# Kernel tuning notes

Hardware: AMD Instinct MI355X
Metric: run time of the kernel (lower is better)

The kernel has to match this reference:

```python
import jax, jax.numpy as jnp
import numpy as np
import math

B, S, D, H, DH, DFF = 2, 2048, 2048, 16, 128, 8192
EPS = 1e-6
K_AMB = -1.0


def log_map_origin(x, K):
    # x: (..., d+1) Lorentz point -> tangent vector (..., d)
    xi = x[..., 1:]
    n = jnp.sqrt(jnp.sum(xi * xi, axis=-1, keepdims=True))
    a = jnp.sqrt(-K) * n
    # asinh(a)/a, stable near 0 (on-manifold, acosh(sqrt(-K)x0) == asinh(sqrt(-K)||xi||))
    f = jnp.where(a < 1e-6, 1.0 - a * a / 6.0, jnp.arcsinh(a) / jnp.maximum(a, 1e-12))
    return f * xi


def exp_map_stable(v, K):
    # v: (..., d) tangent -> Lorentz point (..., d+1); x0 from exact constraint
    n = jnp.sqrt(jnp.sum(v * v, axis=-1, keepdims=True))
    a = jnp.sqrt(-K) * n
    sinc = jnp.where(a < 1e-6, 1.0 + a * a / 6.0, jnp.sinh(a) / jnp.maximum(a, 1e-12))
    xi = sinc * v
    x0 = jnp.sqrt(-1.0 / K + jnp.sum(xi * xi, axis=-1, keepdims=True))
    return jnp.concatenate([x0, xi], axis=-1)


def lorentz_rmsnorm(x, scale):
    v = log_map_origin(x, K_AMB)
    rms = jnp.sqrt(jnp.mean(v * v, axis=-1, keepdims=True) + EPS)
    return exp_map_stable(scale * (v / rms), K_AMB)


def per_head_attention(x_normed, mask, Wq, Wk, Wv, Wo, head_K):
    v = log_map_origin(x_normed, K_AMB)  # (B,S,D)
    def split(w):
        return (v @ w).reshape(B, S, H, DH).transpose(0, 2, 1, 3)  # (B,H,S,DH)
    q, k, vv = split(Wq), split(Wk), split(Wv)
    Kh = head_K[None, :, None, None]  # (1,H,1,1) per-head curvature
    ql = exp_map_stable(q, Kh)  # (B,H,S,DH+1)
    kl = exp_map_stable(k, Kh)
    # Lorentz inner product <q,k>_L = -q0 k0 + qi.ki via signed metric
    metric = jnp.concatenate([-jnp.ones((1,)), jnp.ones((DH,))])
    L = jnp.einsum('bhqd,bhkd->bhqk', ql * metric, kl)
    # negative squared-distance proxy: 2<q,k>_L - 2/K  (zero when q==k)
    scores = (2.0 * L - 2.0 / Kh) / math.sqrt(DH)
    scores = jnp.where(mask[None, None, :, :], scores, -1e30)
    attn = jax.nn.softmax(scores, axis=-1)
    out = jnp.einsum('bhqk,bhkd->bhqd', attn, vv)  # (B,H,S,DH)
    out = out.transpose(0, 2, 1, 3).reshape(B, S, H * DH)
    return out @ Wo  # Euclidean (B,S,D)


def block_forward(x, mask, scale1, scale2, Wq, Wk, Wv, Wo, head_K, W1, W2):
    xn = lorentz_rmsnorm(x, scale1)
    attn_out = per_head_attention(xn, mask, Wq, Wk, Wv, Wo, head_K)
    x = exp_map_stable(log_map_origin(x, K_AMB) + attn_out, K_AMB)
    xn = lorentz_rmsnorm(x, scale2)
    vf = log_map_origin(xn, K_AMB)
    ffn_eu_pre = jax.nn.gelu(vf @ W1, approximate=False) @ W2
    ffn_out = exp_map_stable(ffn_eu_pre, K_AMB)
    x = exp_map_stable(log_map_origin(x, K_AMB) + log_map_origin(ffn_out, K_AMB), K_AMB)
    return x


def setup_inputs() -> dict:
    key = jax.random.key(0)
    ks = jax.random.split(key, 9)
    v0 = jax.random.normal(ks[0], (B, S, D), jnp.float32) * 0.02
    x = exp_map_stable(v0, K_AMB)  # on-manifold input (B,S,D+1)
    mask = jnp.tril(jnp.ones((S, S), bool))  # causal: True = attend
    init_scale = 1.0 / math.sqrt(D)
    w_std = 0.02
    return {
        'x': x,
        'mask': mask,
        'scale1': jnp.full((D,), init_scale, jnp.float32),
        'scale2': jnp.full((D,), init_scale, jnp.float32),
        'Wq': jax.random.normal(ks[1], (D, H * DH), jnp.float32) * w_std,
        'Wk': jax.random.normal(ks[2], (D, H * DH), jnp.float32) * w_std,
        'Wv': jax.random.normal(ks[3], (D, H * DH), jnp.float32) * w_std,
        'Wo': jax.random.normal(ks[4], (H * DH, D), jnp.float32) * w_std,
        'head_K': jnp.full((H,), -1.0, jnp.float32),
        'W1': jax.random.normal(ks[5], (D, DFF), jnp.float32) * w_std,
        'W2': jax.random.normal(ks[6], (DFF, D), jnp.float32) * w_std,
    }


def reference(x, mask, scale1, scale2, Wq, Wk, Wv, Wo, head_K, W1, W2):
    return block_forward(x, mask, scale1, scale2, Wq, Wk, Wv, Wo, head_K, W1, W2)
```

## Files before the change

### kernel.cpp

```cpp
#include <hip/hip_runtime.h>
#include <stdint.h>

typedef unsigned short u16;
typedef __attribute__((ext_vector_type(8))) short bf16x8;
typedef __attribute__((ext_vector_type(4))) float f32x4;

#define SEQ    2048
#define NB     2
#define NHEAD  16
#define DHEAD  128
#define DMODEL 2048
#define DFFN   8192
#define MROWS  4096

__device__ __forceinline__ u16 f2bf(float x) {
  union { float f; uint32_t u; } v; v.f = x;
  return (u16)((v.u + 0x7fffu + ((v.u >> 16) & 1u)) >> 16);
}
__device__ __forceinline__ float bf2f(u16 h) {
  union { uint32_t u; float f; } v; v.u = ((uint32_t)h) << 16;
  return v.f;
}
__device__ __forceinline__ void gload16(const void* g, void* l) {
  __builtin_amdgcn_global_load_lds((const __attribute__((address_space(1))) void*)g,
                                   (__attribute__((address_space(3))) void*)l,
                                   16, 0, 0);
}
__device__ __forceinline__ float blockSum256(float v) {
  __shared__ float red[4];
  #pragma unroll
  for (int m = 1; m < 64; m <<= 1) v += __shfl_xor(v, m, 64);
  int w = threadIdx.x >> 6;
  if ((threadIdx.x & 63) == 0) red[w] = v;
  __syncthreads();
  float s = red[0] + red[1] + red[2] + red[3];
  __syncthreads();
  return s;
}

__global__ void transpose_w(const float* __restrict__ in, u16* __restrict__ out, int R, int C) {
  __shared__ float tile[32][33];
  int c0 = blockIdx.x * 32, r0 = blockIdx.y * 32;
  int tx = threadIdx.x, ty = threadIdx.y;
  #pragma unroll
  for (int i = 0; i < 4; ++i)
    tile[ty + 8*i][tx] = in[(size_t)(r0 + ty + 8*i) * C + c0 + tx];
  __syncthreads();
  #pragma unroll
  for (int i = 0; i < 4; ++i)
    out[(size_t)(c0 + ty + 8*i) * R + r0 + tx] = f2bf(tile[tx][ty + 8*i]);
}

__global__ void ln_first(const float* __restrict__ x, const float* __restrict__ scale,
                         float* __restrict__ v1, u16* __restrict__ t1) {
  int row = blockIdx.x;
  const float* xr = x + (size_t)row * (DMODEL + 1) + 1;
  float vals[8]; float ss = 0.f;
  #pragma unroll
  for (int i = 0; i < 8; ++i) {
    int idx = threadIdx.x + 256 * i;
    vals[i] = xr[idx];
    ss += vals[i] * vals[i];
  }
  ss = blockSum256(ss);
  float n = sqrtf(ss);
  float f = (n < 1e-6f) ? (1.0f - n * n * (1.0f/6.0f)) : (asinhf(n) / n);
  float rms = sqrtf(f * f * ss * (1.0f / DMODEL) + 1e-6f);
  float ir = 1.0f / rms;
  #pragma unroll
  for (int i = 0; i < 8; ++i) {
    int idx = threadIdx.x + 256 * i;
    float v = f * vals[i];
    v1[(size_t)row * DMODEL + idx] = v;
    t1[(size_t)row * DMODEL + idx] = f2bf(scale[idx] * v * ir);
  }
}

__global__ void rms_mid3(float* __restrict__ u, const float* __restrict__ p0,
                         const float* __restrict__ p1, const float* __restrict__ scale,
                         u16* __restrict__ t) {
  int row = blockIdx.x;
  size_t base = (size_t)row * DMODEL;
  float vals[8]; float ss = 0.f;
  #pragma unroll
  for (int i = 0; i < 8; ++i) {
    int idx = threadIdx.x + 256*i;
    float v = u[base + idx] + p0[base + idx] + p1[base + idx];
    vals[i] = v; ss += v*v;
  }
  ss = blockSum256(ss);
  float ir = 1.0f / sqrtf(ss * (1.0f / DMODEL) + 1e-6f);
  #pragma unroll
  for (int i = 0; i < 8; ++i) {
    int idx = threadIdx.x + 256*i;
    u[base + idx] = vals[i];
    t[base + idx] = f2bf(scale[idx]*vals[i]*ir);
  }
}

__global__ void final_exp3(const float* __restrict__ u, const float* __restrict__ p0,
                           const float* __restrict__ p1, float* __restrict__ out) {
  int row = blockIdx.x;
  size_t base = (size_t)row * DMODEL;
  float vals[8]; float ss = 0.f;
  #pragma unroll
  for (int i = 0; i < 8; ++i) {
    int idx = threadIdx.x + 256*i;
    float v = u[base + idx] + p0[base + idx] + p1[base + idx];
    vals[i] = v; ss += v*v;
  }
  ss = blockSum256(ss);
  float n = sqrtf(ss);
  float f = (n < 1e-6f) ? (1.0f + n*n*(1.0f/6.0f)) : (sinhf(n)/n);
  float* orow = out + (size_t)row * (DMODEL + 1);
  if (threadIdx.x == 0) orow[0] = sqrtf(1.0f + f*f*ss);
  #pragma unroll
  for (int i = 0; i < 8; ++i) { int idx = threadIdx.x + 256*i; orow[1+idx] = f*vals[i]; }
}

template<int EPI>
__global__ __launch_bounds__(512, 2) void gemm256(
    const u16* __restrict__ A, const u16* __restrict__ Bt,
    u16* __restrict__ Cb, float* Cf,
    int M, int N, int K, int kHalf)
{
  __shared__ __attribute__((aligned(128))) char smem[131072];
  const int tid = threadIdx.x;
  const int w = tid >> 6, lane = tid & 63;
  const int lrow = lane & 15, kq = lane >> 4;
  const int wm = w >> 2, wn = w & 3;

  const int ksel = blockIdx.y;
  A  += (size_t)ksel * kHalf;
  Bt += (size_t)ksel * kHalf;
  if (EPI == 3) Cf += (size_t)ksel * M * N;
  const int NT = kHalf >> 6;

  const int nwg = gridDim.x;
  const int cpx = nwg >> 3;
  const int sid = (blockIdx.x & 7) * cpx + (blockIdx.x >> 3);
  const int NX = N >> 8;
  const int bx = sid % NX, by = sid / NX;
  const int m0 = by * 256, n0 = bx * 256;

  size_t goff[2];
  #pragma unroll
  for (int r = 0; r < 2; ++r) {
    int L = r * 8192 + tid * 16;
    int U = L ^ (((L >> 9) & 1) << 5);
    int si = U >> 10;
    int row = (si >> 1) * 16 + ((U >> 6) & 15);
    int col = (si & 1) * 32 + ((U & 63) >> 1);
    goff[r] = (size_t)row * K + col;
  }
  auto stage_half = [&](const u16* g, int ldsOff) {
    #pragma unroll
    for (int r = 0; r < 2; ++r)
      gload16(g + goff[r], smem + ldsOff + r * 8192 + w * 1024);
  };

  const u16* A0 = A  + (size_t)m0 * K;
  const u16* A1 = A  + (size_t)(m0 + 128) * K;
  const u16* B0 = Bt + (size_t)n0 * K;
  const u16* B1 = Bt + (size_t)(n0 + 128) * K;

  const int aoff = (lrow * 64 + kq * 16) ^ ((lrow & 8) << 2);

  f32x4 acc[8][4] = {};

  stage_half(A0, 0);
  stage_half(A1, 16384);
  stage_half(B0, 32768);
  stage_half(B1, 49152);
  stage_half(A0 + 64, 65536);
  stage_half(A1 + 64, 65536 + 16384);
  asm volatile("s_waitcnt vmcnt(4)" ::: "memory");
  asm volatile("s_barrier" ::: "memory");

  for (int t = 0; t < NT; ++t) {
    const int buf = t & 1;
    const char* ab = smem + buf * 65536 + wm * 16384 + aoff;
    const char* bb = smem + buf * 65536 + 32768 + (wn >> 1) * 16384 + (wn & 1) * 8192 + aoff;
    bf16x8 a0[4][2], a1[4][2], b0[2][2], b1[2][2];

    #pragma unroll
    for (int i = 0; i < 4; ++i)
      #pragma unroll
      for (int kk = 0; kk < 2; ++kk)
        a0[i][kk] = *(const bf16x8*)(ab + (i*2 + kk) * 1024);
    #pragma unroll
    for (int j = 0; j < 2; ++j)
      #pragma unroll
      for (int kk = 0; kk < 2; ++kk)
        b0[j][kk] = *(const bf16x8*)(bb + (j*2 + kk) * 1024);
    if (t + 1 < NT) stage_half(B0 + (t+1)*64, (buf^1)*65536 + 32768);
    asm volatile("s_barrier" ::: "memory");
    __builtin_amdgcn_s_setprio(1);
    #pragma unroll
    for (int kk = 0; kk < 2; ++kk)
      #pragma unroll
      for (int i = 0; i < 4; ++i)
        #pragma unroll
        for (int j = 0; j < 2; ++j)
          acc[i][j] = __builtin_amdgcn_mfma_f32_16x16x32_bf16(a0[i][kk], b0[j][kk], acc[i][j], 0, 0, 0);
    __builtin_amdgcn_s_setprio(0);
    asm volatile("s_barrier" ::: "memory");

    #pragma unroll
    for (int i = 0; i < 4; ++i)
      #pragma unroll
      for (int kk = 0; kk < 2; ++kk)
        a1[i][kk] = *(const bf16x8*)(ab + ((4 + i)*2 + kk) * 1024);
    if (t + 1 < NT) stage_half(B1 + (t+1)*64, (buf^1)*65536 + 49152);
    asm volatile("s_barrier" ::: "memory");
    __builtin_amdgcn_s_setprio(1);
    #pragma unroll
    for (int kk = 0; kk < 2; ++kk)
      #pragma unroll
      for (int i = 0; i < 4; ++i)
        #pragma unroll
        for (int j = 0; j < 2; ++j)
          acc[4 + i][j] = __builtin_amdgcn_mfma_f32_16x16x32_bf16(a1[i][kk], b0[j][kk], acc[4 + i][j], 0, 0, 0);
    __builtin_amdgcn_s_setprio(0);
    asm volatile("s_barrier" ::: "memory");

    #pragma unroll
    for (int j = 0; j < 2; ++j)
      #pragma unroll
      for (int kk = 0; kk < 2; ++kk)
        b1[j][kk] = *(const bf16x8*)(bb + ((2 + j)*2 + kk) * 1024);
    if (t + 2 < NT) stage_half(A0 + (t+2)*64, buf*65536);
    asm volatile("s_barrier" ::: "memory");
    __builtin_amdgcn_s_setprio(1);
    #pragma unroll
    for (int kk = 0; kk < 2; ++kk)
      #pragma unroll
      for (int i = 0; i < 4; ++i)
        #pragma unroll
        for (int j = 0; j < 2; ++j)
          acc[4 + i][2 + j] = __builtin_amdgcn_mfma_f32_16x16x32_bf16(a1[i][kk], b1[j][kk], acc[4 + i][2 + j], 0, 0, 0);
    __builtin_amdgcn_s_setprio(0);
    asm volatile("s_barrier" ::: "memory");

    if (t + 2 < NT) stage_half(A1 + (t+2)*64, buf*65536 + 16384);
    asm volatile("s_barrier" ::: "memory");
    __builtin_amdgcn_s_setprio(1);
    #pragma unroll
    for (int kk = 0; kk < 2; ++kk)
      #pragma unroll
      for (int i = 0; i < 4; ++i)
        #pragma unroll
        for (int j = 0; j < 2; ++j)
          acc[i][2 + j] = __builtin_amdgcn_mfma_f32_16x16x32_bf16(a0[i][kk], b1[j][kk], acc[i][2 + j], 0, 0, 0);
    __builtin_amdgcn_s_setprio(0);
    if (t + 2 < NT) asm volatile("s_waitcnt vmcnt(4)" ::: "memory");
    else            asm volatile("s_waitcnt vmcnt(0)" ::: "memory");
    asm volatile("s_barrier" ::: "memory");
  }

  #pragma unroll
  for (int i = 0; i < 8; ++i)
    #pragma unroll
    for (int j = 0; j < 4; ++j)
      #pragma unroll
      for (int r = 0; r < 4; ++r) {
        int row = m0 + wm*128 + i*16 + kq*4 + r;
        int col = n0 + wn*64 + j*16 + lrow;
        size_t idx = (size_t)row * N + col;
        float v = acc[i][j][r];
        if (EPI == 0) {
          Cb[idx] = f2bf(v);
        } else if (EPI == 3) {
          Cf[idx] = v;
        } else {
          float g = 0.5f * v * (1.0f + erff(v * 0.70710678118654752f));
          Cb[idx] = f2bf(g);
        }
      }
}

__global__ void prep_qk(const u16* __restrict__ in, const float* __restrict__ headK,
                        u16* __restrict__ Lout, float* __restrict__ l0,
                        int instride, int off) {
  int gid = blockIdx.x * 4 + (threadIdx.x >> 6);
  int lane = threadIdx.x & 63;
  int b = gid >> 15;
  int rem = gid & 32767;
  int h = rem >> 11;
  int s = rem & 2047;
  const u16* src = in + ((size_t)(b * SEQ + s)) * instride + off + h * DHEAD + lane * 2;
  float v0 = bf2f(src[0]), v1 = bf2f(src[1]);
  float nn = v0*v0 + v1*v1;
  #pragma unroll
  for (int m = 1; m < 64; m <<= 1) nn += __shfl_xor(nn, m, 64);
  float Kh = headK[h];
  float sk = sqrtf(-Kh);
  float a = sk * sqrtf(nn);
  float f = (a < 1e-6f) ? (1.0f + a*a*(1.0f/6.0f)) : (sinhf(a) / a);
  u16* dst = Lout + (size_t)gid * DHEAD + lane * 2;
  dst[0] = f2bf(f * v0);
  dst[1] = f2bf(f * v1);
  if (lane == 0) l0[gid] = sqrtf(-1.0f/Kh + f*f*nn);
}

__global__ void vtrans(const u16* __restrict__ vb, u16* __restrict__ VT,
                       int instride, int off) {
  __shared__ u16 tile[32][33];
  int bh = blockIdx.x;
  int b = bh >> 4, h = bh & 15;
  int s0 = blockIdx.y * 32, d0 = blockIdx.z * 32;
  int tx = threadIdx.x, ty = threadIdx.y;
  #pragma unroll
  for (int i = 0; i < 4; ++i)
    tile[ty + 8*i][tx] = vb[((size_t)(b*SEQ + s0 + ty + 8*i)) * instride + off + h*DHEAD + d0 + tx];
  __syncthreads();
  #pragma unroll
  for (int i = 0; i < 4; ++i)
    VT[((size_t)bh*DHEAD + d0 + ty + 8*i) * SEQ + s0 + tx] = tile[tx][ty + 8*i];
}

__global__ __launch_bounds__(256, 2) void attn_kernel(
    const u16* __restrict__ Ql, const u16* __restrict__ Kl,
    const u16* __restrict__ VT, const float* __restrict__ ql0,
    const float* __restrict__ kl0, const float* __restrict__ headK,
    u16* __restrict__ out) {
  __shared__ u16 klds[2][32 * 128];
  __shared__ u16 vlds[2][128 * 32];
  __shared__ u16 plds[4][32 * 36];
  const int tid = threadIdx.x, w = tid >> 6, lane = tid & 63;
  const int lrow = lane & 15, kq = lane >> 4;
  const int id = blockIdx.x;
  const int bh = id & 31;
  const int qb = 15 - (id >> 5);
  const int q0 = qb * 128 + w * 32;
  const int b = bh >> 4, h = bh & 15;
  const float Kh = headK[h];
  const float LOG2E = 1.44269504088896f;
  const float isd = 0.088388347648318447f;
  const float sc_mul = 2.0f * isd * LOG2E;
  const float sc_add = (-2.0f / Kh) * isd * LOG2E;

  const u16* kbase  = Kl + (size_t)bh * SEQ * DHEAD;
  const u16* vtbase = VT + (size_t)bh * DHEAD * SEQ;
  const float* kl0b = kl0 + (size_t)bh * SEQ;
  u16* pw = &plds[w][0];

  bf16x8 aq[2][4];
  const u16* qbase = Ql + ((size_t)bh * SEQ + q0) * DHEAD;
  #pragma unroll
  for (int m = 0; m < 2; ++m)
    #pragma unroll
    for (int dc = 0; dc < 4; ++dc)
      aq[m][dc] = *(const bf16x8*)&qbase[(size_t)(m*16 + lrow) * DHEAD + dc*32 + kq*8];
  float q0r[2][4];
  #pragma unroll
  for (int m = 0; m < 2; ++m)
    #pragma unroll
    for (int r = 0; r < 4; ++r)
      q0r[m][r] = ql0[(size_t)bh * SEQ + q0 + m*16 + kq*4 + r];

  auto stage = [&](int k0, int buf) {
    #pragma unroll
    for (int i = 0; i < 2; ++i) {
      int rl = w*8 + i*4 + (lane >> 4);
      int c = (lane & 15) ^ (rl & 15);
      gload16(kbase + ((size_t)(k0 + rl)) * DHEAD + c * 8,
              &klds[buf][(w*8 + i*4) * 128]);
    }
    #pragma unroll
    for (int i = 0; i < 2; ++i) {
      int rl = w*32 + i*16 + (lane >> 2);
      int c = (lane & 3) ^ ((rl >> 1) & 3);
      gload16(vtbase + (size_t)rl * SEQ + k0 + c * 8,
              &vlds[buf][(w*32 + i*16) * 32]);
    }
  };

  float lacc[2][4] = {};
  f32x4 o[2][8] = {};
  const int niter = qb * 4 + 4;

  stage(0, 0);
  for (int i = 0; i < niter; ++i) {
    const int k0 = i * 32, buf = i & 1;
    float kc0 = kl0b[k0 + lrow];
    float kc1 = kl0b[k0 + 16 + lrow];
    if (i + 1 < niter) {
      stage(k0 + 32, buf ^ 1);
      asm volatile("s_waitcnt vmcnt(4)" ::: "memory");
    } else {
      asm volatile("s_waitcnt vmcnt(0)" ::: "memory");
    }
    asm volatile("s_barrier" ::: "memory");

    f32x4 sc[2][2] = {};
    #pragma unroll
    for (int dc = 0; dc < 4; ++dc) {
      int c = dc*4 + kq;
      bf16x8 bk0 = *(const bf16x8*)&klds[buf][lrow*128        + (c ^ (lrow & 15)) * 8];
      bf16x8 bk1 = *(const bf16x8*)&klds[buf][(16 + lrow)*128 + (c ^ ((16 + lrow) & 15)) * 8];
      #pragma unroll
      for (int m = 0; m < 2; ++m) {
        sc[m][0] = __builtin_amdgcn_mfma_f32_16x16x32_bf16(aq[m][dc], bk0, sc[m][0], 0, 0, 0);
        sc[m][1] = __builtin_amdgcn_mfma_f32_16x16x32_bf16(aq[m][dc], bk1, sc[m][1], 0, 0, 0);
      }
    }
    #pragma unroll
    for (int m = 0; m < 2; ++m)
      #pragma unroll
      for (int r = 0; r < 4; ++r) {
        int qg = q0 + m*16 + kq*4 + r;
        float p0 = exp2f((sc[m][0][r] - q0r[m][r] * kc0) * sc_mul + sc_add);
        float p1 = exp2f((sc[m][1][r] - q0r[m][r] * kc1) * sc_mul + sc_add);
        p0 = (k0 + lrow      <= qg) ? p0 : 0.f;
        p1 = (k0 + 16 + lrow <= qg) ? p1 : 0.f;
        lacc[m][r] += p0 + p1;
        pw[(m*16 + kq*4 + r) * 36 + lrow]      = f2bf(p0);
        pw[(m*16 + kq*4 + r) * 36 + 16 + lrow] = f2bf(p1);
      }
    bf16x8 ap0 = *(const bf16x8*)&pw[(size_t)lrow * 36 + kq*8];
    bf16x8 ap1 = *(const bf16x8*)&pw[(size_t)(16 + lrow) * 36 + kq*8];
    int vc = (kq ^ ((lrow >> 1) & 3)) * 8;
    #pragma unroll
    for (int n = 0; n < 8; ++n) {
      bf16x8 bv = *(const bf16x8*)&vlds[buf][(n*16 + lrow) * 32 + vc];
      o[0][n] = __builtin_amdgcn_mfma_f32_16x16x32_bf16(ap0, bv, o[0][n], 0, 0, 0);
      o[1][n] = __builtin_amdgcn_mfma_f32_16x16x32_bf16(ap1, bv, o[1][n], 0, 0, 0);
    }
    asm volatile("s_barrier" ::: "memory");
  }

  float rcl[2][4];
  #pragma unroll
  for (int m = 0; m < 2; ++m)
    #pragma unroll
    for (int r = 0; r < 4; ++r) {
      float s = lacc[m][r];
      #pragma unroll
      for (int mm = 1; mm < 16; mm <<= 1) s += __shfl_xor(s, mm, 16);
      rcl[m][r] = 1.0f / s;
    }
  #pragma unroll
  for (int m = 0; m < 2; ++m)
    #pragma unroll
    for (int n = 0; n < 8; ++n)
      #pragma unroll
      for (int r = 0; r < 4; ++r) {
        int qg = q0 + m*16 + kq*4 + r;
        out[((size_t)b * SEQ + qg) * DMODEL + h * DHEAD + n*16 + lrow] =
            f2bf(o[m][n][r] * rcl[m][r]);
      }
}

extern "C" void kernel_launch(void* const* d_in, const int* in_sizes, int n_in,
                              void* d_out, int out_size, void* d_ws, size_t ws_size,
                              hipStream_t stream) {
  const float* x      = (const float*)d_in[0];
  const float* scale1 = (const float*)d_in[2];
  const float* scale2 = (const float*)d_in[3];
  const float* Wq     = (const float*)d_in[4];
  const float* Wk     = (const float*)d_in[5];
  const float* Wv     = (const float*)d_in[6];
  const float* Wo     = (const float*)d_in[7];
  const float* headK  = (const float*)d_in[8];
  const float* W1     = (const float*)d_in[9];
  const float* W2     = (const float*)d_in[10];
  float* out = (float*)d_out;

  char* p = (char*)d_ws;
  size_t off = 0;
  auto take = [&](size_t bytes) -> char* {
    char* r = p + off;
    off += (bytes + 255) & ~(size_t)255;
    return r;
  };
  u16* WqT = (u16*)take((size_t)DMODEL*DMODEL*2);
  u16* WkT = (u16*)take((size_t)DMODEL*DMODEL*2);
  u16* WvT = (u16*)take((size_t)DMODEL*DMODEL*2);
  u16* WoT = (u16*)take((size_t)DMODEL*DMODEL*2);
  u16* W1T = (u16*)take((size_t)DMODEL*DFFN*2);
  u16* W2T = (u16*)take((size_t)DMODEL*DFFN*2);
  float* vres = (float*)take((size_t)MROWS*DMODEL*4);
  u16* tbuf = (u16*)take((size_t)MROWS*DMODEL*2);
  u16* qkvb = (u16*)take((size_t)MROWS*3*DMODEL*2);
  u16* Qlb  = (u16*)take((size_t)MROWS*DMODEL*2);
  u16* Klb  = (u16*)take((size_t)MROWS*DMODEL*2);
  u16* VTb  = (u16*)take((size_t)MROWS*DMODEL*2);
  float* q0b = (float*)take((size_t)NB*NHEAD*SEQ*4);
  float* k0b = (float*)take((size_t)NB*NHEAD*SEQ*4);
  u16* hbuf = qkvb;
  u16* attnout = tbuf;

  float* PoA = (float*)qkvb;
  float* PoB = PoA + (size_t)MROWS*DMODEL;
  float* PfA = (float*)WqT;
  float* PfB = (float*)Klb;

  dim3 tb(32, 8);
  transpose_w<<<dim3(DMODEL/32, DMODEL/32), tb, 0, stream>>>(Wq, WqT, DMODEL, DMODEL);
  transpose_w<<<dim3(DMODEL/32, DMODEL/32), tb, 0, stream>>>(Wk, WkT, DMODEL, DMODEL);
  transpose_w<<<dim3(DMODEL/32, DMODEL/32), tb, 0, stream>>>(Wv, WvT, DMODEL, DMODEL);
  transpose_w<<<dim3(DMODEL/32, DMODEL/32), tb, 0, stream>>>(Wo, WoT, DMODEL, DMODEL);
  transpose_w<<<dim3(DFFN/32,   DMODEL/32), tb, 0, stream>>>(W1, W1T, DMODEL, DFFN);
  transpose_w<<<dim3(DMODEL/32, DFFN/32),   tb, 0, stream>>>(W2, W2T, DFFN, DMODEL);

  ln_first<<<MROWS, 256, 0, stream>>>(x, scale1, vres, tbuf);

  gemm256<0><<<dim3((3*DMODEL/256)*(MROWS/256), 1), 512, 0, stream>>>(
      tbuf, WqT, qkvb, nullptr, MROWS, 3*DMODEL, DMODEL, DMODEL);

  prep_qk<<<NB*NHEAD*SEQ/4, 256, 0, stream>>>(qkvb, headK, Qlb, q0b, 3*DMODEL, 0);
  prep_qk<<<NB*NHEAD*SEQ/4, 256, 0, stream>>>(qkvb, headK, Klb, k0b, 3*DMODEL, DMODEL);
  vtrans<<<dim3(NB*NHEAD, SEQ/32, DHEAD/32), tb, 0, stream>>>(qkvb, VTb, 3*DMODEL, 2*DMODEL);

  attn_kernel<<<dim3(512), 256, 0, stream>>>(Qlb, Klb, VTb, q0b, k0b, headK, attnout);

  gemm256<3><<<dim3((DMODEL/256)*(MROWS/256), 2), 512, 0, stream>>>(
      attnout, WoT, nullptr, PoA, MROWS, DMODEL, DMODEL, DMODEL/2);

  rms_mid3<<<MROWS, 256, 0, stream>>>(vres, PoA, PoB, scale2, tbuf);

  gemm256<2><<<dim3((DFFN/256)*(MROWS/256), 1), 512, 0, stream>>>(
      tbuf, W1T, hbuf, nullptr, MROWS, DFFN, DMODEL, DMODEL);

  gemm256<3><<<dim3((DMODEL/256)*(MROWS/256), 2), 512, 0, stream>>>(
      hbuf, W2T, nullptr, PfA, MROWS, DMODEL, DFFN, DFFN/2);

  final_exp3<<<MROWS, 256, 0, stream>>>(vres, PfA, (float*)W1T, out);

  (void)PfB; (void)in_sizes; (void)n_in; (void)out_size; (void)ws_size;
}
```

Baseline: 905.1 us.

## Software-pipeline GEMM LDS fragment loads across iterations and cut barriers

The bf16 MFMA GEMM main loop is restructured so the next tile's a0/b0 register fragments are read from LDS at the end of the current iteration. The first fragments are preloaded before the loop. The four MFMA quadrants are reordered (a0·b0, a0·b1, a1·b0, a1·b1), and each iteration now has half as many s_barriers, with adjusted vmcnt/lgkmcnt waits. The aim is to overlap LDS reads and global-to-LDS staging with MFMA work and reduce synchronisation stalls. In exchange it holds more fragment registers live and depends on delicate wait-count ordering. Host pointer aliases for partial buffers are also simplified to equivalent addresses.

```diff
diff --git a/kernel.cpp b/kernel.cpp
--- a/kernel.cpp
+++ b/kernel.cpp
@@ -167,6 +167,7 @@
   const int aoff = (lrow * 64 + kq * 16) ^ ((lrow & 8) << 2);
 
   f32x4 acc[8][4] = {};
+  bf16x8 a0[4][2], a1[4][2], b0[2][2], b1[2][2];
 
   stage_half(A0, 0);
   stage_half(A1, 16384);
@@ -176,25 +177,35 @@
   stage_half(A1 + 64, 65536 + 16384);
   asm volatile("s_waitcnt vmcnt(4)" ::: "memory");
   asm volatile("s_barrier" ::: "memory");
+  {
+    const char* ab = smem + wm * 16384 + aoff;
+    const char* bb = smem + 32768 + (wn >> 1) * 16384 + (wn & 1) * 8192 + aoff;
+    #pragma unroll
+    for (int i = 0; i < 4; ++i)
+      #pragma unroll
+      for (int kk = 0; kk < 2; ++kk)
+        a0[i][kk] = *(const bf16x8*)(ab + (i*2 + kk) * 1024);
+    #pragma unroll
+    for (int j = 0; j < 2; ++j)
+      #pragma unroll
+      for (int kk = 0; kk < 2; ++kk)
+        b0[j][kk] = *(const bf16x8*)(bb + (j*2 + kk) * 1024);
+  }
 
   for (int t = 0; t < NT; ++t) {
     const int buf = t & 1;
-    const char* ab = smem + buf * 65536 + wm * 16384 + aoff;
-    const char* bb = smem + buf * 65536 + 32768 + (wn >> 1) * 16384 + (wn & 1) * 8192 + aoff;
-    bf16x8 a0[4][2], a1[4][2], b0[2][2], b1[2][2];
-
-    #pragma unroll
-    for (int i = 0; i < 4; ++i)
+    const char* ab  = smem + buf * 65536 + wm * 16384 + aoff;
+    const char* bb  = smem + buf * 65536 + 32768 + (wn >> 1) * 16384 + (wn & 1) * 8192 + aoff;
+    const char* abn = smem + (buf^1) * 65536 + wm * 16384 + aoff;
+    const char* bbn = smem + (buf^1) * 65536 + 32768 + (wn >> 1) * 16384 + (wn & 1) * 8192 + aoff;
+
+    asm volatile("s_barrier" ::: "memory");
+    #pragma unroll
+    for (int j = 0; j < 2; ++j)
       #pragma unroll
       for (int kk = 0; kk < 2; ++kk)
-        a0[i][kk] = *(const bf16x8*)(ab + (i*2 + kk) * 1024);
-    #pragma unroll
-    for (int j = 0; j < 2; ++j)
-      #pragma unroll
-      for (int kk = 0; kk < 2; ++kk)
-        b0[j][kk] = *(const bf16x8*)(bb + (j*2 + kk) * 1024);
+        b1[j][kk] = *(const bf16x8*)(bb + ((2 + j)*2 + kk) * 1024);
     if (t + 1 < NT) stage_half(B0 + (t+1)*64, (buf^1)*65536 + 32768);
-    asm volatile("s_barrier" ::: "memory");
     __builtin_amdgcn_s_setprio(1);
     #pragma unroll
     for (int kk = 0; kk < 2; ++kk)
@@ -204,15 +215,27 @@
         for (int j = 0; j < 2; ++j)
           acc[i][j] = __builtin_amdgcn_mfma_f32_16x16x32_bf16(a0[i][kk], b0[j][kk], acc[i][j], 0, 0, 0);
     __builtin_amdgcn_s_setprio(0);
+
     asm volatile("s_barrier" ::: "memory");
-
     #pragma unroll
     for (int i = 0; i < 4; ++i)
       #pragma unroll
       for (int kk = 0; kk < 2; ++kk)
         a1[i][kk] = *(const bf16x8*)(ab + ((4 + i)*2 + kk) * 1024);
     if (t + 1 < NT) stage_half(B1 + (t+1)*64, (buf^1)*65536 + 49152);
+    __builtin_amdgcn_s_setprio(1);
+    #pragma unroll
+    for (int kk = 0; kk < 2; ++kk)
+      #pragma unroll
+      for (int i = 0; i < 4; ++i)
+        #pragma unroll
+        for (int j = 0; j < 2; ++j)
+          acc[i][2 + j] = __builtin_amdgcn_mfma_f32_16x16x32_bf16(a0[i][kk], b1[j][kk], acc[i][2 + j], 0, 0, 0);
+    __builtin_amdgcn_s_setprio(0);
+    asm volatile("s_waitcnt lgkmcnt(0)" ::: "memory");
+
     asm volatile("s_barrier" ::: "memory");
+    if (t + 2 < NT) stage_half(A0 + (t+2)*64, buf*65536);
     __builtin_amdgcn_s_setprio(1);
     #pragma unroll
     for (int kk = 0; kk < 2; ++kk)
@@ -222,15 +245,23 @@
         for (int j = 0; j < 2; ++j)
           acc[4 + i][j] = __builtin_amdgcn_mfma_f32_16x16x32_bf16(a1[i][kk], b0[j][kk], acc[4 + i][j], 0, 0, 0);
     __builtin_amdgcn_s_setprio(0);
+
     asm volatile("s_barrier" ::: "memory");
-
-    #pragma unroll
-    for (int j = 0; j < 2; ++j)
-      #pragma unroll
-      for (int kk = 0; kk < 2; ++kk)
-        b1[j][kk] = *(const bf16x8*)(bb + ((2 + j)*2 + kk) * 1024);
-    if (t + 2 < NT) stage_half(A0 + (t+2)*64, buf*65536);
-    asm volatile("s_barrier" ::: "memory");
+    if (t + 1 < NT) {
+      if (t + 2 < NT) asm volatile("s_waitcnt vmcnt(2)" ::: "memory");
+      else            asm volatile("s_waitcnt vmcnt(0)" ::: "memory");
+      #pragma unroll
+      for (int i = 0; i < 4; ++i)
+        #pragma unroll
+        for (int kk = 0; kk < 2; ++kk)
+          a0[i][kk] = *(const bf16x8*)(abn + (i*2 + kk) * 1024);
+      #pragma unroll
+      for (int j = 0; j < 2; ++j)
+        #pragma unroll
+        for (int kk = 0; kk < 2; ++kk)
+          b0[j][kk] = *(const bf16x8*)(bbn + (j*2 + kk) * 1024);
+    }
+    if (t + 2 < NT) stage_half(A1 + (t+2)*64, buf*65536 + 16384);
     __builtin_amdgcn_s_setprio(1);
     #pragma unroll
     for (int kk = 0; kk < 2; ++kk)
@@ -240,22 +271,6 @@
         for (int j = 0; j < 2; ++j)
           acc[4 + i][2 + j] = __builtin_amdgcn_mfma_f32_16x16x32_bf16(a1[i][kk], b1[j][kk], acc[4 + i][2 + j], 0, 0, 0);
     __builtin_amdgcn_s_setprio(0);
-    asm volatile("s_barrier" ::: "memory");
-
-    if (t + 2 < NT) stage_half(A1 + (t+2)*64, buf*65536 + 16384);
-    asm volatile("s_barrier" ::: "memory");
-    __builtin_amdgcn_s_setprio(1);
-    #pragma unroll
-    for (int kk = 0; kk < 2; ++kk)
-      #pragma unroll
-      for (int i = 0; i < 4; ++i)
-        #pragma unroll
-        for (int j = 0; j < 2; ++j)
-          acc[i][2 + j] = __builtin_amdgcn_mfma_f32_16x16x32_bf16(a0[i][kk], b1[j][kk], acc[i][2 + j], 0, 0, 0);
-    __builtin_amdgcn_s_setprio(0);
-    if (t + 2 < NT) asm volatile("s_waitcnt vmcnt(4)" ::: "memory");
-    else            asm volatile("s_waitcnt vmcnt(0)" ::: "memory");
-    asm volatile("s_barrier" ::: "memory");
   }
 
   #pragma unroll
@@ -492,9 +507,7 @@
   u16* attnout = tbuf;
 
   float* PoA = (float*)qkvb;
-  float* PoB = PoA + (size_t)MROWS*DMODEL;
   float* PfA = (float*)WqT;
-  float* PfB = (float*)Klb;
 
   dim3 tb(32, 8);
   transpose_w<<<dim3(DMODEL/32, DMODEL/32), tb, 0, stream>>>(Wq, WqT, DMODEL, DMODEL);
@@ -518,7 +531,7 @@
   gemm256<3><<<dim3((DMODEL/256)*(MROWS/256), 2), 512, 0, stream>>>(
       attnout, WoT, nullptr, PoA, MROWS, DMODEL, DMODEL, DMODEL/2);
 
-  rms_mid3<<<MROWS, 256, 0, stream>>>(vres, PoA, PoB, scale2, tbuf);
+  rms_mid3<<<MROWS, 256, 0, stream>>>(vres, PoA, PoA + (size_t)MROWS*DMODEL, scale2, tbuf);
 
   gemm256<2><<<dim3((DFFN/256)*(MROWS/256), 1), 512, 0, stream>>>(
       tbuf, W1T, hbuf, nullptr, MROWS, DFFN, DMODEL, DMODEL);
@@ -526,7 +539,7 @@
   gemm256<3><<<dim3((DMODEL/256)*(MROWS/256), 2), 512, 0, stream>>>(
       hbuf, W2T, nullptr, PfA, MROWS, DMODEL, DFFN, DFFN/2);
 
-  final_exp3<<<MROWS, 256, 0, stream>>>(vres, PfA, (float*)W1T, out);
-
-  (void)PfB; (void)in_sizes; (void)n_in; (void)out_size; (void)ws_size;
-}
+  final_exp3<<<MROWS, 256, 0, stream>>>(vres, PfA, PfA + (size_t)MROWS*DMODEL, out);
+
+  (void)in_sizes; (void)n_in; (void)out_size; (void)ws_size;
+}
```

Result: no change. 899.6 us (-0.6%).
